# Optimization experiments

Measured on AMD Instinct MI355X. Metric: run time of the kernel, lower is better.

Reference implementation:

```python
import jax, jax.numpy as jnp
import numpy as np

N = 100000   # nodes
E = 1600000  # edges (avg degree 16)
DIN, DH, DOUT = 128, 128, 64


def setup_inputs() -> dict:
    key = jax.random.key(0)
    ks = jax.random.split(key, 10)
    x = jax.random.normal(ks[0], (N, DIN), dtype=jnp.float32)
    edge_index = jax.random.randint(ks[1], (2, E), 0, N, dtype=jnp.int32)

    def kaiming(k, fan_out, fan_in):
        # kaiming_uniform_ with nonlinearity='relu': bound = sqrt(6/fan_in)
        bound = np.sqrt(6.0 / fan_in)
        return jax.random.uniform(k, (fan_out, fan_in), jnp.float32, -bound, bound)

    W1 = kaiming(ks[2], DH, DIN)
    W2 = kaiming(ks[3], DH, DH)
    W3 = kaiming(ks[4], DH, DH)
    W4 = kaiming(ks[5], DOUT, DH)
    b1 = jnp.zeros((DH,), jnp.float32)
    b2 = jnp.zeros((DH,), jnp.float32)
    b3 = jnp.zeros((DH,), jnp.float32)
    b4 = jnp.zeros((DOUT,), jnp.float32)
    return {"x": x, "edge_index": edge_index,
            "W1": W1, "b1": b1, "W2": W2, "b2": b2,
            "W3": W3, "b3": b3, "W4": W4, "b4": b4}


def reference(x, edge_index, W1, b1, W2, b2, W3, b3, W4, b4):
    n = x.shape[0]
    src, dst = edge_index[0], edge_index[1]
    # gcn_norm with add_self_loops=False: deg = in-degree at dst (unit weights)
    deg = jax.ops.segment_sum(jnp.ones(src.shape[0], x.dtype), dst, num_segments=n)
    deg_inv_sqrt = jnp.where(deg > 0, jax.lax.rsqrt(jnp.maximum(deg, 1.0)) * jnp.sqrt(jnp.maximum(deg, 1.0)) / jnp.maximum(deg, 1.0) * jnp.sqrt(jnp.maximum(deg, 1.0)), 0.0)
    deg_inv_sqrt = jnp.where(deg > 0, 1.0 / jnp.sqrt(jnp.maximum(deg, 1.0)), 0.0)
    norm = deg_inv_sqrt[src] * deg_inv_sqrt[dst]  # [E]

    def gcn_layer(h, W, b):
        h = h @ W.T                                # [n, out] dense transform
        msg = h[src] * norm[:, None]               # gather + scale  [E, out]
        out = jax.ops.segment_sum(msg, dst, num_segments=n)  # scatter-add
        return out + b

    h = jax.nn.relu(gcn_layer(x, W1, b1))
    h = jax.nn.relu(gcn_layer(h, W2, b2))
    h = jax.nn.relu(gcn_layer(h, W3, b3))
    return gcn_layer(h, W4, b4)
```

## Files before the change

### kernel.cpp

```cpp
#include <hip/hip_runtime.h>
#include <hip/hip_bf16.h>

#define CAP 64

typedef __attribute__((ext_vector_type(8))) short bf16x8;
typedef __attribute__((ext_vector_type(4))) float f32x4;
typedef _Float16 f16;
typedef __attribute__((ext_vector_type(2))) _Float16 f16x2;

__device__ __forceinline__ ushort f2bf(float f) {
    uint u = __float_as_uint(f);
    u = u + 0x7FFF + ((u >> 16) & 1);
    return (ushort)(u >> 16);
}
__device__ __forceinline__ float bf2f(ushort b) { return __uint_as_float(((uint)b) << 16); }

__global__ void fill_kernel(const int* __restrict__ src, const int* __restrict__ dst, int E,
                            int* __restrict__ fil, int* __restrict__ csr, int N) {
    const int xg = blockIdx.x & 7;
    const int gidx = blockIdx.x >> 3;
    const int ngrp = gridDim.x >> 3;
    const int lo = xg * (N >> 3);
    const int hi = (xg == 7) ? N : lo + (N >> 3);

    const int nq = E >> 2;
    for (int q = gidx * blockDim.x + threadIdx.x; q < nq; q += ngrp * blockDim.x) {
        const int e = q * 4;
        int4 d4 = *(const int4*)(dst + e);
        int4 s4 = *(const int4*)(src + e);
        if (d4.x >= lo && d4.x < hi) { int p = atomicAdd(&fil[d4.x], 1); if (p < CAP) csr[(size_t)d4.x * CAP + p] = s4.x; }
        if (d4.y >= lo && d4.y < hi) { int p = atomicAdd(&fil[d4.y], 1); if (p < CAP) csr[(size_t)d4.y * CAP + p] = s4.y; }
        if (d4.z >= lo && d4.z < hi) { int p = atomicAdd(&fil[d4.z], 1); if (p < CAP) csr[(size_t)d4.z * CAP + p] = s4.z; }
        if (d4.w >= lo && d4.w < hi) { int p = atomicAdd(&fil[d4.w], 1); if (p < CAP) csr[(size_t)d4.w * CAP + p] = s4.w; }
    }
    if (gidx == 0) {
        for (int e = nq * 4 + (int)threadIdx.x; e < E; e += blockDim.x) {
            int d = dst[e];
            if (d >= lo && d < hi) {
                int p = atomicAdd(&fil[d], 1);
                if (p < CAP) csr[(size_t)d * CAP + p] = src[e];
            }
        }
    }
}

__global__ void dis_kernel(const int* __restrict__ cnt, float* __restrict__ dis, int N) {
    int i = blockIdx.x * blockDim.x + threadIdx.x;
    if (i < N) {
        int c = cnt[i];
        dis[i] = (c > 0) ? rsqrtf((float)c) : 0.0f;
    }
}

__global__ void wconv_kernel(const float* __restrict__ W1, const float* __restrict__ W2,
                             const float* __restrict__ W3, const float* __restrict__ W4,
                             ushort* __restrict__ hilo) {
    int i = blockIdx.x * 256 + threadIdx.x;
    const float* W;
    ushort* hi;
    int off;
    if (i < 16384)      { W = W1; hi = hilo;          off = i; }
    else if (i < 32768) { W = W2; hi = hilo + 32768;  off = i - 16384; }
    else if (i < 49152) { W = W3; hi = hilo + 65536;  off = i - 32768; }
    else                { W = W4; hi = hilo + 98304;  off = i - 49152; }
    float w = W[off];
    ushort h = f2bf(w);
    int span = (i < 49152) ? 16384 : 8192;
    hi[off] = h;
    hi[off + span] = f2bf(w - bf2f(h));
}

template <int COLS>
__global__ __launch_bounds__(256) void mfma_gemm_kernel(const float* __restrict__ F,
                                                        const ushort* __restrict__ Whi,
                                                        const ushort* __restrict__ Wlo,
                                                        const float* __restrict__ dis,
                                                        f16* __restrict__ G, int N) {
    constexpr int CT = COLS / 16;
    const int wave = threadIdx.x >> 6;
    const int lane = threadIdx.x & 63;
    const int lr = lane & 15;
    const int kg = lane >> 4;

    const int rowBase = blockIdx.x * 128 + wave * 32;

    f32x4 acc[2][CT];
#pragma unroll
    for (int rt = 0; rt < 2; ++rt)
#pragma unroll
        for (int c = 0; c < CT; ++c) acc[rt][c] = (f32x4){0.f, 0.f, 0.f, 0.f};

#pragma unroll
    for (int kt = 0; kt < 4; ++kt) {
        bf16x8 Ah[2], Al[2];
#pragma unroll
        for (int rt = 0; rt < 2; ++rt) {
            int row = rowBase + rt * 16 + lr;
            row = row < N ? row : N - 1;
            const float* p = F + (size_t)row * 128 + kt * 32 + kg * 8;
            float4 v0 = *(const float4*)p;
            float4 v1 = *(const float4*)(p + 4);
            float f[8] = {v0.x, v0.y, v0.z, v0.w, v1.x, v1.y, v1.z, v1.w};
            bf16x8 h, l;
#pragma unroll
            for (int j = 0; j < 8; ++j) {
                ushort hb = f2bf(f[j]);
                h[j] = (short)hb;
                l[j] = (short)f2bf(f[j] - bf2f(hb));
            }
            Ah[rt] = h;
            Al[rt] = l;
        }
#pragma unroll
        for (int c = 0; c < CT; ++c) {
            const size_t wo = (size_t)(c * 16 + lr) * 128 + kt * 32 + kg * 8;
            bf16x8 Bh = *(const bf16x8*)(Whi + wo);
            bf16x8 Bl = *(const bf16x8*)(Wlo + wo);
#pragma unroll
            for (int rt = 0; rt < 2; ++rt) {
                acc[rt][c] = __builtin_amdgcn_mfma_f32_16x16x32_bf16(Al[rt], Bh, acc[rt][c], 0, 0, 0);
                acc[rt][c] = __builtin_amdgcn_mfma_f32_16x16x32_bf16(Ah[rt], Bl, acc[rt][c], 0, 0, 0);
                acc[rt][c] = __builtin_amdgcn_mfma_f32_16x16x32_bf16(Ah[rt], Bh, acc[rt][c], 0, 0, 0);
            }
        }
    }

#pragma unroll
    for (int rt = 0; rt < 2; ++rt) {
#pragma unroll
        for (int j = 0; j < 4; ++j) {
            int row = rowBase + rt * 16 + kg * 4 + j;
            if (row < N) {
                float d = dis[row];
#pragma unroll
                for (int c = 0; c < CT; ++c)
                    G[(size_t)row * COLS + c * 16 + lr] = (f16)(acc[rt][c][j] * d);
            }
        }
    }
}

template <int WIDTH, bool DO_RELU>
__global__ __launch_bounds__(256) void agg_kernel(const f16* __restrict__ g,
                                                  const int* __restrict__ csr,
                                                  const int* __restrict__ cnt,
                                                  const float* __restrict__ dis,
                                                  const float* __restrict__ bias,
                                                  float* __restrict__ out, int N) {
    constexpr int VPL = WIDTH / 64;
    int node = blockIdx.x * 4 + (threadIdx.x >> 6);
    if (node >= N) return;
    int lane = threadIdx.x & 63;

    int c = cnt[node];
    if (c > CAP) c = CAP;
    const int* lst = csr + (size_t)node * CAP;
    float acc0 = 0.f, acc1 = 0.f;

    int j = 0;
    for (; j + 8 <= c; j += 8) {
        int4 sA = *(const int4*)(lst + j);
        int4 sB = *(const int4*)(lst + j + 4);
        if (VPL == 2) {
            f16x2 t0 = *(const f16x2*)(g + (size_t)sA.x * WIDTH + lane * 2);
            f16x2 t1 = *(const f16x2*)(g + (size_t)sA.y * WIDTH + lane * 2);
            f16x2 t2 = *(const f16x2*)(g + (size_t)sA.z * WIDTH + lane * 2);
            f16x2 t3 = *(const f16x2*)(g + (size_t)sA.w * WIDTH + lane * 2);
            f16x2 t4 = *(const f16x2*)(g + (size_t)sB.x * WIDTH + lane * 2);
            f16x2 t5 = *(const f16x2*)(g + (size_t)sB.y * WIDTH + lane * 2);
            f16x2 t6 = *(const f16x2*)(g + (size_t)sB.z * WIDTH + lane * 2);
            f16x2 t7 = *(const f16x2*)(g + (size_t)sB.w * WIDTH + lane * 2);
            acc0 += (((float)t0[0] + (float)t1[0]) + ((float)t2[0] + (float)t3[0])) +
                    (((float)t4[0] + (float)t5[0]) + ((float)t6[0] + (float)t7[0]));
            acc1 += (((float)t0[1] + (float)t1[1]) + ((float)t2[1] + (float)t3[1])) +
                    (((float)t4[1] + (float)t5[1]) + ((float)t6[1] + (float)t7[1]));
        } else {
            float u0 = (float)g[(size_t)sA.x * WIDTH + lane];
            float u1 = (float)g[(size_t)sA.y * WIDTH + lane];
            float u2 = (float)g[(size_t)sA.z * WIDTH + lane];
            float u3 = (float)g[(size_t)sA.w * WIDTH + lane];
            float u4 = (float)g[(size_t)sB.x * WIDTH + lane];
            float u5 = (float)g[(size_t)sB.y * WIDTH + lane];
            float u6 = (float)g[(size_t)sB.z * WIDTH + lane];
            float u7 = (float)g[(size_t)sB.w * WIDTH + lane];
            acc0 += ((u0 + u1) + (u2 + u3)) + ((u4 + u5) + (u6 + u7));
        }
    }
    for (; j + 4 <= c; j += 4) {
        int4 sA = *(const int4*)(lst + j);
        if (VPL == 2) {
            f16x2 t0 = *(const f16x2*)(g + (size_t)sA.x * WIDTH + lane * 2);
            f16x2 t1 = *(const f16x2*)(g + (size_t)sA.y * WIDTH + lane * 2);
            f16x2 t2 = *(const f16x2*)(g + (size_t)sA.z * WIDTH + lane * 2);
            f16x2 t3 = *(const f16x2*)(g + (size_t)sA.w * WIDTH + lane * 2);
            acc0 += ((float)t0[0] + (float)t1[0]) + ((float)t2[0] + (float)t3[0]);
            acc1 += ((float)t0[1] + (float)t1[1]) + ((float)t2[1] + (float)t3[1]);
        } else {
            float u0 = (float)g[(size_t)sA.x * WIDTH + lane];
            float u1 = (float)g[(size_t)sA.y * WIDTH + lane];
            float u2 = (float)g[(size_t)sA.z * WIDTH + lane];
            float u3 = (float)g[(size_t)sA.w * WIDTH + lane];
            acc0 += (u0 + u1) + (u2 + u3);
        }
    }
    for (; j < c; ++j) {
        int s = lst[j];
        if (VPL == 2) {
            f16x2 t = *(const f16x2*)(g + (size_t)s * WIDTH + lane * 2);
            acc0 += (float)t[0];
            acc1 += (float)t[1];
        } else {
            acc0 += (float)g[(size_t)s * WIDTH + lane];
        }
    }

    float d = dis[node];
    if (VPL == 2) {
        float v0 = fmaf(d, acc0, bias[lane * 2 + 0]);
        float v1 = fmaf(d, acc1, bias[lane * 2 + 1]);
        if (DO_RELU) { v0 = fmaxf(v0, 0.f); v1 = fmaxf(v1, 0.f); }
        float2 o = make_float2(v0, v1);
        *(float2*)(out + (size_t)node * WIDTH + lane * 2) = o;
    } else {
        float v0 = fmaf(d, acc0, bias[lane]);
        if (DO_RELU) v0 = fmaxf(v0, 0.f);
        out[(size_t)node * WIDTH + lane] = v0;
    }
}

extern "C" void kernel_launch(void* const* d_in, const int* in_sizes, int n_in,
                              void* d_out, int out_size, void* d_ws, size_t ws_size,
                              hipStream_t stream) {
    const float* x  = (const float*)d_in[0];
    const int*   ei = (const int*)d_in[1];
    const float* W1 = (const float*)d_in[2];
    const float* b1 = (const float*)d_in[3];
    const float* W2 = (const float*)d_in[4];
    const float* b2 = (const float*)d_in[5];
    const float* W3 = (const float*)d_in[6];
    const float* b3 = (const float*)d_in[7];
    const float* W4 = (const float*)d_in[8];
    const float* b4 = (const float*)d_in[9];

    const int N = in_sizes[0] / 128;
    const int E = in_sizes[1] / 2;
    const int* src = ei;
    const int* dst = ei + E;

    char* w = (char*)d_ws;
    float* F   = (float*)w; w += (size_t)N * 128 * 4;
    f16*   G   = (f16*)w;   w += (size_t)N * 128 * 4;
    int*   csr = (int*)w;   w += (size_t)N * CAP * 4;
    float* dis = (float*)w; w += (size_t)N * 4;
    int*   fil = (int*)w;   w += (size_t)N * 4;
    ushort* Whl = (ushort*)w; w += (16384 * 6 + 8192 * 2) * 2;
    ushort* Whi1 = Whl;          ushort* Wlo1 = Whl + 16384;
    ushort* Whi2 = Whl + 32768;  ushort* Wlo2 = Whl + 49152;
    ushort* Whi3 = Whl + 65536;  ushort* Wlo3 = Whl + 81920;
    ushort* Whi4 = Whl + 98304;  ushort* Wlo4 = Whl + 106496;

    float* out = (float*)d_out;

    hipMemsetAsync(fil, 0, (size_t)N * sizeof(int), stream);

    fill_kernel<<<2048, 256, 0, stream>>>(src, dst, E, fil, csr, N);
    dis_kernel<<<(N + 255) / 256, 256, 0, stream>>>(fil, dis, N);
    wconv_kernel<<<224, 256, 0, stream>>>(W1, W2, W3, W4, Whl);

    const int gemm_grid = (N + 127) / 128;
    const int agg_grid  = (N + 3) / 4;

    mfma_gemm_kernel<128><<<gemm_grid, 256, 0, stream>>>(x, Whi1, Wlo1, dis, G, N);
    agg_kernel<128, true><<<agg_grid, 256, 0, stream>>>(G, csr, fil, dis, b1, F, N);
    mfma_gemm_kernel<128><<<gemm_grid, 256, 0, stream>>>(F, Whi2, Wlo2, dis, G, N);
    agg_kernel<128, true><<<agg_grid, 256, 0, stream>>>(G, csr, fil, dis, b2, F, N);
    mfma_gemm_kernel<128><<<gemm_grid, 256, 0, stream>>>(F, Whi3, Wlo3, dis, G, N);
    agg_kernel<128, true><<<agg_grid, 256, 0, stream>>>(G, csr, fil, dis, b3, F, N);
    mfma_gemm_kernel<64><<<gemm_grid, 256, 0, stream>>>(F, Whi4, Wlo4, dis, G, N);
    agg_kernel<64, false><<<agg_grid, 256, 0, stream>>>(G, csr, fil, dis, b4, out, N);
}
```

Measured before the change: 589.0 us.

## Pre-bucket edges by destination range before CSR fill, merge prep kernels

The CSR build used to have every fill block scan all edges and keep only those in its destination range, so the edge list was read eight times. A new route kernel reads the edges once and packs each one (source shifted left by 14, destination offset) into one of eight destination-range buckets, stored in the G workspace. The fill kernel then reads only its own bucket. Weight conversion and degree-normalisation are merged into one launch. The 14-bit packing assumes each bucket range is at most 16384 nodes and source indices fit in 18 bits, and buckets are capped at BCAP entries.

```diff
diff --git a/kernel.cpp b/kernel.cpp
--- a/kernel.cpp
+++ b/kernel.cpp
@@ -2,6 +2,7 @@
 #include <hip/hip_bf16.h>
 
 #define CAP 64
+#define BCAP 250000
 
 typedef __attribute__((ext_vector_type(8))) short bf16x8;
 typedef __attribute__((ext_vector_type(4))) float f32x4;
@@ -15,59 +16,108 @@
 }
 __device__ __forceinline__ float bf2f(ushort b) { return __uint_as_float(((uint)b) << 16); }
 
-__global__ void fill_kernel(const int* __restrict__ src, const int* __restrict__ dst, int E,
-                            int* __restrict__ fil, int* __restrict__ csr, int N) {
+__device__ __forceinline__ int bkt(int d, int r) {
+    int b = 0;
+    if (d >= 4 * r) b = 4;
+    if (d >= (b + 2) * r) b += 2;
+    if (d >= (b + 1) * r) b += 1;
+    return b;
+}
+
+__global__ __launch_bounds__(256) void route_kernel(const int* __restrict__ src,
+                                                    const int* __restrict__ dst,
+                                                    int E, int N,
+                                                    uint* __restrict__ buf,
+                                                    int* __restrict__ gcur) {
+    __shared__ int lcnt[8], lbase[8];
+    if (threadIdx.x < 8) lcnt[threadIdx.x] = 0;
+    __syncthreads();
+    const int r = (N + 7) >> 3;
+    const int e = (blockIdx.x * 256 + threadIdx.x) * 4;
+    int bb[4]; uint pk[4]; int ne = 0;
+    if (e + 4 <= E) {
+        int4 d4 = *(const int4*)(dst + e);
+        int4 s4 = *(const int4*)(src + e);
+        int ds[4] = {d4.x, d4.y, d4.z, d4.w};
+        int ss[4] = {s4.x, s4.y, s4.z, s4.w};
+#pragma unroll
+        for (int k = 0; k < 4; ++k) {
+            int d = ds[k];
+            int b = bkt(d, r);
+            bb[k] = b;
+            pk[k] = ((uint)ss[k] << 14) | (uint)(d - b * r);
+            atomicAdd(&lcnt[b], 1);
+        }
+        ne = 4;
+    } else {
+        for (int t = e; t < E; ++t) {
+            int d = dst[t];
+            int b = bkt(d, r);
+            bb[ne] = b;
+            pk[ne] = ((uint)src[t] << 14) | (uint)(d - b * r);
+            atomicAdd(&lcnt[b], 1);
+            ++ne;
+        }
+    }
+    __syncthreads();
+    if (threadIdx.x < 8) {
+        lbase[threadIdx.x] = atomicAdd(&gcur[threadIdx.x], lcnt[threadIdx.x]);
+        lcnt[threadIdx.x] = 0;
+    }
+    __syncthreads();
+    for (int k = 0; k < ne; ++k) {
+        int idx = lbase[bb[k]] + atomicAdd(&lcnt[bb[k]], 1);
+        if (idx < BCAP) buf[(size_t)bb[k] * BCAP + idx] = pk[k];
+    }
+}
+
+__global__ __launch_bounds__(256) void fill_kernel(const uint* __restrict__ buf,
+                                                   const int* __restrict__ gcur,
+                                                   int* __restrict__ fil,
+                                                   int* __restrict__ csr, int N) {
     const int xg = blockIdx.x & 7;
     const int gidx = blockIdx.x >> 3;
     const int ngrp = gridDim.x >> 3;
-    const int lo = xg * (N >> 3);
-    const int hi = (xg == 7) ? N : lo + (N >> 3);
-
-    const int nq = E >> 2;
-    for (int q = gidx * blockDim.x + threadIdx.x; q < nq; q += ngrp * blockDim.x) {
-        const int e = q * 4;
-        int4 d4 = *(const int4*)(dst + e);
-        int4 s4 = *(const int4*)(src + e);
-        if (d4.x >= lo && d4.x < hi) { int p = atomicAdd(&fil[d4.x], 1); if (p < CAP) csr[(size_t)d4.x * CAP + p] = s4.x; }
-        if (d4.y >= lo && d4.y < hi) { int p = atomicAdd(&fil[d4.y], 1); if (p < CAP) csr[(size_t)d4.y * CAP + p] = s4.y; }
-        if (d4.z >= lo && d4.z < hi) { int p = atomicAdd(&fil[d4.z], 1); if (p < CAP) csr[(size_t)d4.z * CAP + p] = s4.z; }
-        if (d4.w >= lo && d4.w < hi) { int p = atomicAdd(&fil[d4.w], 1); if (p < CAP) csr[(size_t)d4.w * CAP + p] = s4.w; }
-    }
-    if (gidx == 0) {
-        for (int e = nq * 4 + (int)threadIdx.x; e < E; e += blockDim.x) {
-            int d = dst[e];
-            if (d >= lo && d < hi) {
-                int p = atomicAdd(&fil[d], 1);
-                if (p < CAP) csr[(size_t)d * CAP + p] = src[e];
-            }
-        }
-    }
-}
-
-__global__ void dis_kernel(const int* __restrict__ cnt, float* __restrict__ dis, int N) {
-    int i = blockIdx.x * blockDim.x + threadIdx.x;
-    if (i < N) {
-        int c = cnt[i];
-        dis[i] = (c > 0) ? rsqrtf((float)c) : 0.0f;
-    }
-}
-
-__global__ void wconv_kernel(const float* __restrict__ W1, const float* __restrict__ W2,
-                             const float* __restrict__ W3, const float* __restrict__ W4,
-                             ushort* __restrict__ hilo) {
-    int i = blockIdx.x * 256 + threadIdx.x;
-    const float* W;
-    ushort* hi;
-    int off;
-    if (i < 16384)      { W = W1; hi = hilo;          off = i; }
-    else if (i < 32768) { W = W2; hi = hilo + 32768;  off = i - 16384; }
-    else if (i < 49152) { W = W3; hi = hilo + 65536;  off = i - 32768; }
-    else                { W = W4; hi = hilo + 98304;  off = i - 49152; }
-    float w = W[off];
-    ushort h = f2bf(w);
-    int span = (i < 49152) ? 16384 : 8192;
-    hi[off] = h;
-    hi[off + span] = f2bf(w - bf2f(h));
+    const int r = (N + 7) >> 3;
+    const int lo = xg * r;
+    int cnt = gcur[xg];
+    if (cnt > BCAP) cnt = BCAP;
+    const uint* b = buf + (size_t)xg * BCAP;
+    for (int i = gidx * 256 + threadIdx.x; i < cnt; i += ngrp * 256) {
+        uint pk = b[i];
+        int d = lo + (int)(pk & 0x3FFFu);
+        int s = (int)(pk >> 14);
+        int p = atomicAdd(&fil[d], 1);
+        if (p < CAP) csr[(size_t)d * CAP + p] = s;
+    }
+}
+
+__global__ void prep_kernel(const float* __restrict__ W1, const float* __restrict__ W2,
+                            const float* __restrict__ W3, const float* __restrict__ W4,
+                            ushort* __restrict__ hilo,
+                            const int* __restrict__ cnt, float* __restrict__ dis, int N) {
+    int blk = blockIdx.x;
+    if (blk < 224) {
+        int i = blk * 256 + threadIdx.x;
+        const float* W;
+        ushort* hi;
+        int off;
+        if (i < 16384)      { W = W1; hi = hilo;          off = i; }
+        else if (i < 32768) { W = W2; hi = hilo + 32768;  off = i - 16384; }
+        else if (i < 49152) { W = W3; hi = hilo + 65536;  off = i - 32768; }
+        else                { W = W4; hi = hilo + 98304;  off = i - 49152; }
+        float w = W[off];
+        ushort h = f2bf(w);
+        int span = (i < 49152) ? 16384 : 8192;
+        hi[off] = h;
+        hi[off + span] = f2bf(w - bf2f(h));
+    } else {
+        int i = (blk - 224) * 256 + threadIdx.x;
+        if (i < N) {
+            int c = cnt[i];
+            dis[i] = (c > 0) ? rsqrtf((float)c) : 0.0f;
+        }
+    }
 }
 
 template <int COLS>
@@ -252,20 +302,23 @@
     f16*   G   = (f16*)w;   w += (size_t)N * 128 * 4;
     int*   csr = (int*)w;   w += (size_t)N * CAP * 4;
     float* dis = (float*)w; w += (size_t)N * 4;
-    int*   fil = (int*)w;   w += (size_t)N * 4;
+    int*   fil = (int*)w;   w += (size_t)(N + 8) * 4;
+    int*   gcur = fil + N;
     ushort* Whl = (ushort*)w; w += (16384 * 6 + 8192 * 2) * 2;
     ushort* Whi1 = Whl;          ushort* Wlo1 = Whl + 16384;
     ushort* Whi2 = Whl + 32768;  ushort* Wlo2 = Whl + 49152;
     ushort* Whi3 = Whl + 65536;  ushort* Wlo3 = Whl + 81920;
     ushort* Whi4 = Whl + 98304;  ushort* Wlo4 = Whl + 106496;
+    uint* buf = (uint*)G;
 
     float* out = (float*)d_out;
 
-    hipMemsetAsync(fil, 0, (size_t)N * sizeof(int), stream);
-
-    fill_kernel<<<2048, 256, 0, stream>>>(src, dst, E, fil, csr, N);
-    dis_kernel<<<(N + 255) / 256, 256, 0, stream>>>(fil, dis, N);
-    wconv_kernel<<<224, 256, 0, stream>>>(W1, W2, W3, W4, Whl);
+    hipMemsetAsync(fil, 0, (size_t)(N + 8) * sizeof(int), stream);
+
+    const int nq = (E + 3) / 4;
+    route_kernel<<<(nq + 255) / 256, 256, 0, stream>>>(src, dst, E, N, buf, gcur);
+    fill_kernel<<<2048, 256, 0, stream>>>(buf, gcur, fil, csr, N);
+    prep_kernel<<<224 + (N + 255) / 256, 256, 0, stream>>>(W1, W2, W3, W4, Whl, fil, dis, N);
 
     const int gemm_grid = (N + 127) / 128;
     const int agg_grid  = (N + 3) / 4;
```

Result: slower. 604.8 us (+2.7%).
